# Optimization experiments

Hardware: AMD Instinct MI355X
Metric: run time of the kernel (lower is better)

Reference implementation:

```python
import jax, jax.numpy as jnp
import numpy as np

B, S = 32, 256          # sequences, tokens per sequence (prefill)
DIM, NH, NKV, HD = 2048, 16, 16, 128
CLS, GRID, BASE = 1, 16, 10000


def precompute_freqs_cis_2d(grid_size, n_elem, base, cls_token_num):
    half = n_elem // 2
    freqs = 1.0 / (base ** (np.arange(0, half, 2)[: half // 2].astype(np.float32) / half))
    t = np.arange(grid_size, dtype=np.float32)
    fr = np.outer(t, freqs)                      # [grid, half//2]
    fg = np.concatenate([
        np.broadcast_to(fr[:, None, :], (grid_size, grid_size, fr.shape[1])),
        np.broadcast_to(fr[None, :, :], (grid_size, grid_size, fr.shape[1])),
    ], axis=-1)                                  # [grid, grid, half]
    cache = np.stack([np.cos(fg), np.sin(fg)], axis=-1).reshape(grid_size * grid_size, half, 2)
    cond = np.concatenate([np.zeros((cls_token_num, half, 2), np.float32), cache.astype(np.float32)], axis=0)
    return jnp.asarray(cond)                     # [cls+grid^2, half, 2]

FREQS = precompute_freqs_cis_2d(GRID, HD, BASE, CLS)


def _apply_rope(x, fc):
    # x: [T, H, HD], fc: [T, HD//2, 2]
    xr = x.reshape(x.shape[0], x.shape[1], HD // 2, 2)
    c = fc[:, None, :, 0]
    s = fc[:, None, :, 1]
    out = jnp.stack([xr[..., 0] * c - xr[..., 1] * s,
                     xr[..., 1] * c + xr[..., 0] * s], axis=-1)
    return out.reshape(x.shape)


def setup_inputs() -> dict:
    key = jax.random.key(0)
    k1, k2, k3 = jax.random.split(key, 3)
    x = jax.random.normal(k1, (B * S, DIM), dtype=jnp.float32)
    positions = jnp.tile(jnp.arange(S, dtype=jnp.int32), B)  # per-seq positions 0..S-1
    total_kv = (NH + 2 * NKV) * HD
    wqkv = jax.random.normal(k2, (total_kv, DIM), dtype=jnp.float32) * 0.02
    wo = jax.random.normal(k3, (DIM, DIM), dtype=jnp.float32) * 0.02
    return {"x": x, "positions": positions, "wqkv": wqkv, "wo": wo}


def reference(x, positions, wqkv, wo):
    T = x.shape[0]
    kv_size = NKV * HD
    qkv = x @ wqkv.T                               # [T, dim + 2*kv_size]
    xq, xk, xv = jnp.split(qkv, [DIM, DIM + kv_size], axis=-1)
    q = xq.reshape(T, NH, HD)
    k = xk.reshape(T, NKV, HD)
    v = xv.reshape(T, NKV, HD)

    fc = FREQS[positions]                          # [T, HD//2, 2]
    q = _apply_rope(q, fc)
    k = _apply_rope(k, fc)

    # paged attention (prefill): causal attention within each sequence
    qb = q.reshape(B, S, NH, HD)
    kb = k.reshape(B, S, NKV, HD)
    vb = v.reshape(B, S, NKV, HD)
    scale = HD ** -0.5
    scores = jnp.einsum("bqhd,bkhd->bhqk", qb, kb) * scale   # [B,H,S,S]
    causal = jnp.tril(jnp.ones((S, S), dtype=bool))
    scores = jnp.where(causal[None, None], scores, jnp.finfo(scores.dtype).min)
    attn = jax.nn.softmax(scores, axis=-1)
    out = jnp.einsum("bhqk,bkhd->bqhd", attn, vb).reshape(T, DIM)
    return out @ wo.T
```

## Files before the change

kernel.cpp:

```cpp
#include <hip/hip_runtime.h>
#include <cstddef>


typedef float    f32x4 __attribute__((ext_vector_type(4)));
typedef _Float16 f16x8 __attribute__((ext_vector_type(8)));
typedef _Float16 f16x4 __attribute__((ext_vector_type(4)));

#define LOG2E 1.4426950408889634f

__device__ static inline f32x4 mfma16x32(f16x8 a, f16x8 b, f32x4 c) {
  return __builtin_amdgcn_mfma_f32_16x16x32_f16(a, b, c, 0, 0, 0);
}

__device__ static inline void gload16(const void* g, void* lds) {
  __builtin_amdgcn_global_load_lds(
      (const __attribute__((address_space(1))) unsigned int*)g,
      (__attribute__((address_space(3))) unsigned int*)lds, 16, 0, 0);
}

#define BAR()    asm volatile("s_barrier" ::: "memory")
#define VMCNT6() asm volatile("s_waitcnt vmcnt(6)" ::: "memory")

__global__ void cvt_f32_f16(const float* __restrict__ src,
                            _Float16* __restrict__ dst, int n4) {
  int i = blockIdx.x * blockDim.x + threadIdx.x;
  if (i >= n4) return;
  f32x4 v = *(const f32x4*)(src + (size_t)i * 4);
  f16x4 o;
  o[0] = (_Float16)v[0]; o[1] = (_Float16)v[1];
  o[2] = (_Float16)v[2]; o[3] = (_Float16)v[3];
  *(f16x4*)(dst + (size_t)i * 4) = o;
}

template <typename OutT>
__global__ void __launch_bounds__(512, 2)
gemm_bt3(const _Float16* __restrict__ A, const _Float16* __restrict__ Bt,
         OutT* __restrict__ C, int M, int N, int K) {
  __shared__ __attribute__((aligned(16))) _Float16 Ab[2][256 * 64];
  __shared__ __attribute__((aligned(16))) _Float16 Bb[2][256 * 64];

  const int tid  = threadIdx.x;
  const int lane = tid & 63;
  const int w    = tid >> 6;
  const int wm   = w >> 2, wn = w & 3;
  const int g    = lane >> 4, li = lane & 15;

  const int nwg = (int)gridDim.x;
  const int cpx = nwg >> 3;
  const int bid = (int)blockIdx.x;
  const int swz = (bid & 7) * cpx + (bid >> 3);
  const int nbn = N >> 8;
  const int bm  = (swz / nbn) << 8;
  const int bn  = (swz % nbn) << 8;
  const int NT  = K >> 6;

  const int srow = tid >> 3;
  const int scol = ((tid & 7) ^ (srow & 7)) * 8;
  const _Float16* gA = A  + (size_t)(bm + srow) * K + scol;
  const _Float16* gB = Bt + (size_t)(bn + srow) * K + scol;
  const int sdst = w * 1024;

  auto stage = [&](const _Float16* gbase, _Float16* lbase, int h, int kt) {
    const _Float16* gp = gbase + (size_t)h * 128 * K + kt;
    char* lp = (char*)lbase + h * 16384;
#pragma unroll
    for (int j = 0; j < 2; ++j)
      gload16(gp + (size_t)j * 64 * K, lp + j * 8192 + sdst);
  };

  auto rdfrag = [&](const _Float16* buf, int row, int k2) -> f16x8 {
    const int pc = ((k2 << 2) + g) ^ (li & 7);
    return *(const f16x8*)((const char*)buf + row * 128 + pc * 16);
  };

  f32x4 acc[8][4] = {};

  stage(gA, Ab[0], 0, 0);
  stage(gB, Bb[0], 0, 0);
  stage(gB, Bb[0], 1, 0);
  stage(gA, Ab[0], 1, 0);
  stage(gA, Ab[1], 0, (NT > 1) ? 64 : 0);
  VMCNT6();
  BAR();

  for (int T = 0; T < NT; ++T) {
    const int cb = T & 1, nb = cb ^ 1;
    const _Float16* Ac = Ab[cb];
    const _Float16* Bc = Bb[cb];
    const int ktN  = (T + 1 < NT) ? (T + 1) << 6 : 0;
    const int ktN2 = (T + 2 < NT) ? (T + 2) << 6 : 0;

    f16x8 af0[4][2], af1[4][2], bf0[2][2], bf1[2][2];

#pragma unroll
    for (int m = 0; m < 4; ++m)
#pragma unroll
      for (int k2 = 0; k2 < 2; ++k2)
        af0[m][k2] = rdfrag(Ac, wm * 128 + m * 16 + li, k2);
#pragma unroll
    for (int n = 0; n < 2; ++n)
#pragma unroll
      for (int k2 = 0; k2 < 2; ++k2)
        bf0[n][k2] = rdfrag(Bc, wn * 64 + n * 16 + li, k2);
    stage(gB, Bb[nb], 0, ktN);
    BAR();
    __builtin_amdgcn_s_setprio(1);
#pragma unroll
    for (int m = 0; m < 4; ++m)
#pragma unroll
      for (int n = 0; n < 2; ++n)
#pragma unroll
        for (int k2 = 0; k2 < 2; ++k2)
          acc[m][n] = mfma16x32(af0[m][k2], bf0[n][k2], acc[m][n]);
    __builtin_amdgcn_s_setprio(0);
    VMCNT6();
    BAR();

#pragma unroll
    for (int n = 0; n < 2; ++n)
#pragma unroll
      for (int k2 = 0; k2 < 2; ++k2)
        bf1[n][k2] = rdfrag(Bc, wn * 64 + (n + 2) * 16 + li, k2);
    stage(gB, Bb[nb], 1, ktN);
    BAR();
    __builtin_amdgcn_s_setprio(1);
#pragma unroll
    for (int m = 0; m < 4; ++m)
#pragma unroll
      for (int n = 0; n < 2; ++n)
#pragma unroll
        for (int k2 = 0; k2 < 2; ++k2)
          acc[m][n + 2] = mfma16x32(af0[m][k2], bf1[n][k2], acc[m][n + 2]);
    __builtin_amdgcn_s_setprio(0);
    VMCNT6();
    BAR();

#pragma unroll
    for (int m = 0; m < 4; ++m)
#pragma unroll
      for (int k2 = 0; k2 < 2; ++k2)
        af1[m][k2] = rdfrag(Ac, wm * 128 + (m + 4) * 16 + li, k2);
    stage(gA, Ab[nb], 1, ktN);
    BAR();
    __builtin_amdgcn_s_setprio(1);
#pragma unroll
    for (int m = 0; m < 4; ++m)
#pragma unroll
      for (int n = 0; n < 2; ++n)
#pragma unroll
        for (int k2 = 0; k2 < 2; ++k2)
          acc[m + 4][n] = mfma16x32(af1[m][k2], bf0[n][k2], acc[m + 4][n]);
    __builtin_amdgcn_s_setprio(0);
    VMCNT6();
    BAR();

    stage(gA, Ab[cb], 0, ktN2);
    BAR();
    __builtin_amdgcn_s_setprio(1);
#pragma unroll
    for (int m = 0; m < 4; ++m)
#pragma unroll
      for (int n = 0; n < 2; ++n)
#pragma unroll
        for (int k2 = 0; k2 < 2; ++k2)
          acc[m + 4][n + 2] = mfma16x32(af1[m][k2], bf1[n][k2], acc[m + 4][n + 2]);
    __builtin_amdgcn_s_setprio(0);
    VMCNT6();
    BAR();
  }

  asm volatile("s_waitcnt vmcnt(0)" ::: "memory");

#pragma unroll
  for (int m = 0; m < 8; ++m)
#pragma unroll
    for (int n = 0; n < 4; ++n)
#pragma unroll
      for (int r = 0; r < 4; ++r) {
        const int row = bm + wm * 128 + m * 16 + g * 4 + r;
        const int col = bn + wn * 64 + n * 16 + li;
        C[(size_t)row * N + col] = (OutT)acc[m][n][r];
      }
}

__global__ void rope_kernel(_Float16* __restrict__ qkv,
                            const int* __restrict__ positions) {
  const int idx = blockIdx.x * blockDim.x + threadIdx.x;
  const int ch = idx & 15;
  const int hh = (idx >> 4) & 31;
  const int t  = idx >> 9;
  _Float16* p = qkv + (size_t)t * 6144 + hh * 128 + ch * 8;
  const int pos = positions[t];
  f16x8 v = *(const f16x8*)p;
  f16x8 o;
  if (pos == 0) {
#pragma unroll
    for (int u = 0; u < 8; ++u) o[u] = (_Float16)0.f;
  } else {
    const int gi = pos - 1;
    const float tv = (ch < 8) ? (float)(gi >> 4) : (float)(gi & 15);
#pragma unroll
    for (int u = 0; u < 4; ++u) {
      const int k2 = (ch * 4 + u) & 31;
      const float freq = exp2f((float)k2 * (-13.287712379549449f / 32.0f));
      const float ang = tv * freq;
      float s, c;
      sincosf(ang, &s, &c);
      const float x0 = (float)v[2 * u];
      const float x1 = (float)v[2 * u + 1];
      o[2 * u]     = (_Float16)(x0 * c - x1 * s);
      o[2 * u + 1] = (_Float16)(x1 * c + x0 * s);
    }
  }
  *(f16x8*)p = o;
}

__global__ void __launch_bounds__(512)
attn_kernel(const _Float16* __restrict__ qkv, _Float16* __restrict__ O) {
  const int b  = blockIdx.x >> 4;
  const int h  = blockIdx.x & 15;
  const int tb = b << 8;
  const int tid = threadIdx.x;
  const int lane = tid & 63;
  const int w = tid >> 6;
  const int g = lane >> 4, li = lane & 15;

  __shared__ __attribute__((aligned(16))) _Float16 Ks[64 * 128];
  __shared__ __attribute__((aligned(16))) _Float16 Vt[128 * 64];
  __shared__ __attribute__((aligned(16))) _Float16 Ps[8][32 * 40];

  f16x8 qf[2][4];
#pragma unroll
  for (int rb = 0; rb < 2; ++rb)
#pragma unroll
    for (int ks = 0; ks < 4; ++ks)
      qf[rb][ks] = *(const f16x8*)(qkv + (size_t)(tb + w * 32 + rb * 16 + li) * 6144
                                   + h * 128 + ks * 32 + g * 8);

  f32x4 oacc[2][8] = {};
  float m_r[2][4], l_r[2][4];
#pragma unroll
  for (int rb = 0; rb < 2; ++rb)
#pragma unroll
    for (int r = 0; r < 4; ++r) { m_r[rb][r] = -1e30f; l_r[rb][r] = 0.f; }

  const float scale = 0.08838834764831845f;

  for (int kt = 0; kt < 4; ++kt) {
#pragma unroll
    for (int i = 0; i < 2; ++i) {
      const int s = i * 512 + tid;
      const int key = s >> 4;
      const int sch = (s & 15) ^ (key & 7);
      const _Float16* gk = qkv + (size_t)(tb + kt * 64 + key) * 6144
                           + 2048 + h * 128 + sch * 8;
      gload16(gk, (char*)Ks + (i * 512 + (tid & ~63)) * 16);
    }
#pragma unroll
    for (int i = 0; i < 2; ++i) {
      const int s = i * 512 + tid;
      const int key = s >> 4;
      const int chv = s & 15;
      f16x8 v = *(const f16x8*)(qkv + (size_t)(tb + kt * 64 + key) * 6144
                                + 4096 + h * 128 + chv * 8);
#pragma unroll
      for (int e = 0; e < 8; ++e) {
        const int d = chv * 8 + e;
        const int blk = ((key >> 3) ^ (d & 7) ^ ((d >> 3) & 7)) & 7;
        Vt[d * 64 + blk * 8 + (key & 7)] = v[e];
      }
    }
    __syncthreads();

    if (kt <= (w >> 1)) {
      f32x4 sacc[2][4] = {};
#pragma unroll
      for (int ks = 0; ks < 4; ++ks) {
        f16x8 kf[4];
#pragma unroll
        for (int cb = 0; cb < 4; ++cb) {
          const int key = cb * 16 + li;
          const int chunk = (ks * 4 + g) ^ (key & 7);
          kf[cb] = *(const f16x8*)((const char*)Ks + key * 256 + chunk * 16);
        }
#pragma unroll
        for (int rb = 0; rb < 2; ++rb)
#pragma unroll
          for (int cb = 0; cb < 4; ++cb)
            sacc[rb][cb] = mfma16x32(qf[rb][ks], kf[cb], sacc[rb][cb]);
      }
#pragma unroll
      for (int rb = 0; rb < 2; ++rb) {
#pragma unroll
        for (int r = 0; r < 4; ++r) {
          const int q = w * 32 + rb * 16 + g * 4 + r;
          float mx = -1e30f;
#pragma unroll
          for (int cb = 0; cb < 4; ++cb) {
            float sv = sacc[rb][cb][r] * scale;
            const int key = kt * 64 + cb * 16 + li;
            sv = (key <= q) ? sv : -1e30f;
            sacc[rb][cb][r] = sv;
            mx = fmaxf(mx, sv);
          }
#pragma unroll
          for (int off = 1; off < 16; off <<= 1)
            mx = fmaxf(mx, __shfl_xor(mx, off));
          const float mold = m_r[rb][r];
          const float mnew = fmaxf(mold, mx);
          const float alpha = exp2f((mold - mnew) * LOG2E);
          float rsum = 0.f;
#pragma unroll
          for (int cb = 0; cb < 4; ++cb) {
            const float pv = exp2f((sacc[rb][cb][r] - mnew) * LOG2E);
            sacc[rb][cb][r] = pv;
            rsum += pv;
          }
#pragma unroll
          for (int off = 1; off < 16; off <<= 1)
            rsum += __shfl_xor(rsum, off);
          m_r[rb][r] = mnew;
          l_r[rb][r] = l_r[rb][r] * alpha + rsum;
#pragma unroll
          for (int db = 0; db < 8; ++db)
            oacc[rb][db][r] *= alpha;
        }
      }
#pragma unroll
      for (int ks2 = 0; ks2 < 2; ++ks2) {
#pragma unroll
        for (int rb = 0; rb < 2; ++rb)
#pragma unroll
          for (int cbh = 0; cbh < 2; ++cbh) {
            const int cb = ks2 * 2 + cbh;
#pragma unroll
            for (int r = 0; r < 4; ++r)
              Ps[w][(rb * 16 + g * 4 + r) * 40 + cbh * 16 + li] =
                  (_Float16)sacc[rb][cb][r];
          }
        asm volatile("s_waitcnt lgkmcnt(0)" ::: "memory");
        f16x8 pa[2];
#pragma unroll
        for (int rb = 0; rb < 2; ++rb)
          pa[rb] = *(const f16x8*)(&Ps[w][(rb * 16 + li) * 40 + g * 8]);
#pragma unroll
        for (int db = 0; db < 8; ++db) {
          const int d = db * 16 + li;
          const int keych = ks2 * 4 + g;
          const int blk = (keych ^ (d & 7) ^ ((d >> 3) & 7)) & 7;
          const f16x8 vf = *(const f16x8*)(&Vt[d * 64 + blk * 8]);
#pragma unroll
          for (int rb = 0; rb < 2; ++rb)
            oacc[rb][db] = mfma16x32(pa[rb], vf, oacc[rb][db]);
        }
      }
    }
    __syncthreads();
  }
#pragma unroll
  for (int rb = 0; rb < 2; ++rb)
#pragma unroll
    for (int db = 0; db < 8; ++db)
#pragma unroll
      for (int r = 0; r < 4; ++r) {
        const int row = tb + w * 32 + rb * 16 + g * 4 + r;
        const int col = h * 128 + db * 16 + li;
        O[(size_t)row * 2048 + col] = (_Float16)(oacc[rb][db][r] / l_r[rb][r]);
      }
}

extern "C" void kernel_launch(void* const* d_in, const int* in_sizes, int n_in,
                              void* d_out, int out_size, void* d_ws, size_t ws_size,
                              hipStream_t stream) {
  const float* x         = (const float*)d_in[0];
  const int*   positions = (const int*)d_in[1];
  const float* wqkv      = (const float*)d_in[2];
  const float* wo        = (const float*)d_in[3];
  float* out = (float*)d_out;

  char* ws = (char*)d_ws;
  _Float16* qkv    = (_Float16*)(ws);
  _Float16* xf     = (_Float16*)(ws + 100663296);
  _Float16* wqkvf  = (_Float16*)(ws + 134217728);
  _Float16* wof    = (_Float16*)(ws + 159383552);
  _Float16* of     = xf;

  cvt_f32_f16<<<16384, 256, 0, stream>>>(x, xf, 4194304);
  cvt_f32_f16<<<12288, 256, 0, stream>>>(wqkv, wqkvf, 3145728);
  cvt_f32_f16<<< 4096, 256, 0, stream>>>(wo, wof, 1048576);

  gemm_bt3<_Float16><<<768, 512, 0, stream>>>(xf, wqkvf, qkv, 8192, 6144, 2048);

  rope_kernel<<<16384, 256, 0, stream>>>(qkv, positions);

  attn_kernel<<<512, 512, 0, stream>>>(qkv, of);

  gemm_bt3<float><<<256, 512, 0, stream>>>(of, wof, out, 8192, 2048, 2048);
}
```

Baseline: 382.1 us.

## Fuse RoPE into QKV GEMM epilogue and balance causal attention rows

Removes the separate RoPE kernel and applies the rotation inside the QKV GEMM epilogue, exchanging pair partners with a lane shuffle and using fast sincos. This saves a full read and write pass over the Q and K portions of the qkv buffer. The attention kernel now gives each wave one early and one late 16-row query block (w and 15-w), so causal work is spread evenly across waves instead of being concentrated on the last ones. The trade-offs are extra epilogue work in the GEMM and lower-precision __sincosf in place of sincosf.

Measured after the change: 377.8 us. Within noise of the previous version (-1.1%).

```diff
diff --git a/kernel.cpp b/kernel.cpp
--- a/kernel.cpp
+++ b/kernel.cpp
@@ -7,6 +7,7 @@
 typedef _Float16 f16x4 __attribute__((ext_vector_type(4)));
 
 #define LOG2E 1.4426950408889634f
+#define NLOG2B_32 (-0.41524101186192697f)
 
 __device__ static inline f32x4 mfma16x32(f16x8 a, f16x8 b, f32x4 c) {
   return __builtin_amdgcn_mfma_f32_16x16x32_f16(a, b, c, 0, 0, 0);
@@ -32,10 +33,11 @@
   *(f16x4*)(dst + (size_t)i * 4) = o;
 }
 
-template <typename OutT>
+template <typename OutT, bool ROPE>
 __global__ void __launch_bounds__(512, 2)
 gemm_bt3(const _Float16* __restrict__ A, const _Float16* __restrict__ Bt,
-         OutT* __restrict__ C, int M, int N, int K) {
+         OutT* __restrict__ C, int M, int N, int K,
+         const int* __restrict__ positions) {
   __shared__ __attribute__((aligned(16))) _Float16 Ab[2][256 * 64];
   __shared__ __attribute__((aligned(16))) _Float16 Bb[2][256 * 64];
 
@@ -171,48 +173,47 @@
 
   asm volatile("s_waitcnt vmcnt(0)" ::: "memory");
 
-#pragma unroll
-  for (int m = 0; m < 8; ++m)
-#pragma unroll
-    for (int n = 0; n < 4; ++n)
-#pragma unroll
-      for (int r = 0; r < 4; ++r) {
-        const int row = bm + wm * 128 + m * 16 + g * 4 + r;
-        const int col = bn + wn * 64 + n * 16 + li;
-        C[(size_t)row * N + col] = (OutT)acc[m][n][r];
-      }
-}
-
-__global__ void rope_kernel(_Float16* __restrict__ qkv,
-                            const int* __restrict__ positions) {
-  const int idx = blockIdx.x * blockDim.x + threadIdx.x;
-  const int ch = idx & 15;
-  const int hh = (idx >> 4) & 31;
-  const int t  = idx >> 9;
-  _Float16* p = qkv + (size_t)t * 6144 + hh * 128 + ch * 8;
-  const int pos = positions[t];
-  f16x8 v = *(const f16x8*)p;
-  f16x8 o;
-  if (pos == 0) {
-#pragma unroll
-    for (int u = 0; u < 8; ++u) o[u] = (_Float16)0.f;
-  } else {
-    const int gi = pos - 1;
-    const float tv = (ch < 8) ? (float)(gi >> 4) : (float)(gi & 15);
-#pragma unroll
-    for (int u = 0; u < 4; ++u) {
-      const int k2 = (ch * 4 + u) & 31;
-      const float freq = exp2f((float)k2 * (-13.287712379549449f / 32.0f));
-      const float ang = tv * freq;
-      float s, c;
-      sincosf(ang, &s, &c);
-      const float x0 = (float)v[2 * u];
-      const float x1 = (float)v[2 * u + 1];
-      o[2 * u]     = (_Float16)(x0 * c - x1 * s);
-      o[2 * u + 1] = (_Float16)(x1 * c + x0 * s);
+  const bool doRope = ROPE && (bn < 4096);
+  float freqn[4], half2n[4];
+  if (doRope) {
+#pragma unroll
+    for (int n = 0; n < 4; ++n) {
+      const int col = bn + wn * 64 + n * 16 + li;
+      const int d2  = (col >> 1) & 63;
+      freqn[n]  = exp2f((float)(d2 & 31) * NLOG2B_32);
+      half2n[n] = (d2 < 32) ? 1.0f : 0.0f;
     }
   }
-  *(f16x8*)p = o;
+#pragma unroll
+  for (int m = 0; m < 8; ++m) {
+#pragma unroll
+    for (int r = 0; r < 4; ++r) {
+      const int row = bm + wm * 128 + m * 16 + g * 4 + r;
+      float tvA = 0.f, tvB = 0.f;
+      bool zero = false;
+      if (doRope) {
+        const int pos = positions[row];
+        zero = (pos == 0);
+        const int gi = pos - 1;
+        tvA = (float)(gi >> 4);
+        tvB = (float)(gi & 15);
+      }
+#pragma unroll
+      for (int n = 0; n < 4; ++n) {
+        float val = acc[m][n][r];
+        if (doRope) {
+          const float tv  = half2n[n] != 0.f ? tvA : tvB;
+          float s, c;
+          __sincosf(tv * freqn[n], &s, &c);
+          if (zero) { s = 0.f; c = 0.f; }
+          const float partner = __shfl_xor(val, 1);
+          val = val * c + partner * ((li & 1) ? s : -s);
+        }
+        const int col = bn + wn * 64 + n * 16 + li;
+        C[(size_t)row * N + col] = (OutT)val;
+      }
+    }
+  }
 }
 
 __global__ void __launch_bounds__(512)
@@ -229,12 +230,16 @@
   __shared__ __attribute__((aligned(16))) _Float16 Vt[128 * 64];
   __shared__ __attribute__((aligned(16))) _Float16 Ps[8][32 * 40];
 
+  const int qb[2]   = {w, 15 - w};
+  const int qrow[2] = {qb[0] * 16, qb[1] * 16};
+  const int kmax[2] = {qb[0] >> 2, qb[1] >> 2};
+
   f16x8 qf[2][4];
 #pragma unroll
   for (int rb = 0; rb < 2; ++rb)
 #pragma unroll
     for (int ks = 0; ks < 4; ++ks)
-      qf[rb][ks] = *(const f16x8*)(qkv + (size_t)(tb + w * 32 + rb * 16 + li) * 6144
+      qf[rb][ks] = *(const f16x8*)(qkv + (size_t)(tb + qrow[rb] + li) * 6144
                                    + h * 128 + ks * 32 + g * 8);
 
   f32x4 oacc[2][8] = {};
@@ -272,7 +277,8 @@
     }
     __syncthreads();
 
-    if (kt <= (w >> 1)) {
+    const bool act[2] = {kt <= kmax[0], kt <= kmax[1]};
+    if (act[0] || act[1]) {
       f32x4 sacc[2][4] = {};
 #pragma unroll
       for (int ks = 0; ks < 4; ++ks) {
@@ -285,15 +291,17 @@
         }
 #pragma unroll
         for (int rb = 0; rb < 2; ++rb)
-#pragma unroll
-          for (int cb = 0; cb < 4; ++cb)
-            sacc[rb][cb] = mfma16x32(qf[rb][ks], kf[cb], sacc[rb][cb]);
+          if (act[rb])
+#pragma unroll
+            for (int cb = 0; cb < 4; ++cb)
+              sacc[rb][cb] = mfma16x32(qf[rb][ks], kf[cb], sacc[rb][cb]);
       }
 #pragma unroll
       for (int rb = 0; rb < 2; ++rb) {
+        if (!act[rb]) continue;
 #pragma unroll
         for (int r = 0; r < 4; ++r) {
-          const int q = w * 32 + rb * 16 + g * 4 + r;
+          const int q = qrow[rb] + g * 4 + r;
           float mx = -1e30f;
 #pragma unroll
           for (int cb = 0; cb < 4; ++cb) {
@@ -329,7 +337,8 @@
 #pragma unroll
       for (int ks2 = 0; ks2 < 2; ++ks2) {
 #pragma unroll
-        for (int rb = 0; rb < 2; ++rb)
+        for (int rb = 0; rb < 2; ++rb) {
+          if (!act[rb]) continue;
 #pragma unroll
           for (int cbh = 0; cbh < 2; ++cbh) {
             const int cb = ks2 * 2 + cbh;
@@ -338,11 +347,13 @@
               Ps[w][(rb * 16 + g * 4 + r) * 40 + cbh * 16 + li] =
                   (_Float16)sacc[rb][cb][r];
           }
+        }
         asm volatile("s_waitcnt lgkmcnt(0)" ::: "memory");
         f16x8 pa[2];
 #pragma unroll
         for (int rb = 0; rb < 2; ++rb)
-          pa[rb] = *(const f16x8*)(&Ps[w][(rb * 16 + li) * 40 + g * 8]);
+          if (act[rb])
+            pa[rb] = *(const f16x8*)(&Ps[w][(rb * 16 + li) * 40 + g * 8]);
 #pragma unroll
         for (int db = 0; db < 8; ++db) {
           const int d = db * 16 + li;
@@ -351,7 +362,8 @@
           const f16x8 vf = *(const f16x8*)(&Vt[d * 64 + blk * 8]);
 #pragma unroll
           for (int rb = 0; rb < 2; ++rb)
-            oacc[rb][db] = mfma16x32(pa[rb], vf, oacc[rb][db]);
+            if (act[rb])
+              oacc[rb][db] = mfma16x32(pa[rb], vf, oacc[rb][db]);
         }
       }
     }
@@ -363,7 +375,7 @@
     for (int db = 0; db < 8; ++db)
 #pragma unroll
       for (int r = 0; r < 4; ++r) {
-        const int row = tb + w * 32 + rb * 16 + g * 4 + r;
+        const int row = tb + qrow[rb] + g * 4 + r;
         const int col = h * 128 + db * 16 + li;
         O[(size_t)row * 2048 + col] = (_Float16)(oacc[rb][db][r] / l_r[rb][r]);
       }
@@ -389,11 +401,11 @@
   cvt_f32_f16<<<12288, 256, 0, stream>>>(wqkv, wqkvf, 3145728);
   cvt_f32_f16<<< 4096, 256, 0, stream>>>(wo, wof, 1048576);
 
-  gemm_bt3<_Float16><<<768, 512, 0, stream>>>(xf, wqkvf, qkv, 8192, 6144, 2048);
-
-  rope_kernel<<<16384, 256, 0, stream>>>(qkv, positions);
+  gemm_bt3<_Float16, true><<<768, 512, 0, stream>>>(
+      xf, wqkvf, qkv, 8192, 6144, 2048, positions);
 
   attn_kernel<<<512, 512, 0, stream>>>(qkv, of);
 
-  gemm_bt3<float><<<256, 512, 0, stream>>>(of, wof, out, 8192, 2048, 2048);
-}
+  gemm_bt3<float, false><<<256, 512, 0, stream>>>(
+      of, wof, out, 8192, 2048, 2048, nullptr);
+}
```
